# Optimization experiments

Hardware: AMD Instinct MI355X
Metric: run time of the kernel (lower is better)

## Reference

```python
import jax, jax.numpy as jnp
import numpy as np

D_MODEL = 2048
HIDDEN = 2048
NUM_EXPERTS = 8
TOP_K = 2
CAPACITY_FACTOR = 1.25


def setup_inputs() -> dict:
    key = jax.random.key(0)
    k1, k2, k3, k4, k5, k6 = jax.random.split(key, 6)
    N = 8192
    x = jax.random.normal(k1, (N, D_MODEL), dtype=jnp.float32)
    expert_weights = jax.random.uniform(k2, (N, TOP_K), dtype=jnp.float32)
    expert_indices = jax.random.randint(k3, (N, TOP_K), 0, NUM_EXPERTS)
    scale = 0.02
    w1 = jax.random.normal(k4, (NUM_EXPERTS, D_MODEL, HIDDEN), dtype=jnp.float32) * scale
    w3 = jax.random.normal(k5, (NUM_EXPERTS, D_MODEL, HIDDEN), dtype=jnp.float32) * scale
    w2 = jax.random.normal(k6, (NUM_EXPERTS, HIDDEN, D_MODEL), dtype=jnp.float32) * scale
    return {"x": x, "expert_weights": expert_weights, "expert_indices": expert_indices,
            "w1": w1, "w2": w2, "w3": w3}


def reference(x, expert_weights, expert_indices, w1, w2, w3):
    N, top_k = expert_weights.shape
    E = NUM_EXPERTS
    d = x.shape[-1]
    capacity = int(CAPACITY_FACTOR * top_k * N / E)  # expert_capacity()

    flat_idx = expert_indices.reshape(-1)            # (T,) T = N*top_k
    flat_w = expert_weights.reshape(-1)
    T = flat_idx.shape[0]

    # indices_and_bins: histogram + sort (jnp.argsort is stable)
    counts = jax.ops.segment_sum(jnp.ones((T,), dtype=jnp.int32), flat_idx, num_segments=E)
    order = jnp.argsort(flat_idx)                    # sorted assignment order
    sorted_e = flat_idx[order]                       # expert id per sorted slot
    starts = jnp.concatenate([jnp.zeros((1,), jnp.int32), jnp.cumsum(counts)[:-1].astype(jnp.int32)])
    off = jnp.arange(T, dtype=jnp.int32) - starts[sorted_e]  # position within expert bin
    valid = off < capacity                           # capacity dropping
    off_c = jnp.where(valid, off, 0)
    tok = order // top_k                             # source token per assignment

    # binned_gather -> (E, capacity, d); dropped/unfilled slots are zero
    xg = jnp.zeros((E, capacity, d), dtype=x.dtype)
    xg = xg.at[sorted_e, off_c].add(x[tok] * valid[:, None].astype(x.dtype))

    # per-expert SwiGLU MLP (grouped GEMMs)
    h = jax.nn.silu(jnp.einsum('ecd,edh->ech', xg, w1)) * jnp.einsum('ecd,edh->ech', xg, w3)
    y = jnp.einsum('ech,ehd->ecd', h, w2)

    # binned_scatter with expert_weights (weighted combine back to tokens)
    vals = y[sorted_e, off_c] * (flat_w[order] * valid.astype(x.dtype))[:, None]
    out = jnp.zeros((N, d), dtype=x.dtype).at[tok].add(vals)
    return out, counts
```

## Files before the change

kernel.cpp:

```cpp
#include <hip/hip_runtime.h>
#include <hip/hip_bf16.h>
#include <stdint.h>

#define NTOK 8192
#define DM 2048
#define DH 2048
#define NEXP 8
#define TOPK 2
#define TASSIGN (NTOK * TOPK)
#define CAP 2560
#define MROWS (NEXP * CAP)
#define BMTILES 10

using bf16x8 = __attribute__((ext_vector_type(8))) __bf16;
using bf16x2 = __attribute__((ext_vector_type(2))) __bf16;
using f32x4  = __attribute__((ext_vector_type(4))) float;

__device__ __forceinline__ void load_lds16(const void* g, void* l) {
    __builtin_amdgcn_global_load_lds((const __attribute__((address_space(1))) void*)g,
                                     (__attribute__((address_space(3))) void*)l,
                                     16, 0, 0);
}

__global__ void routing_kernel(const int* __restrict__ eidx,
                               int* __restrict__ counts,
                               int* __restrict__ slot_token,
                               int* __restrict__ assign_slot,
                               float* __restrict__ counts_out)
{
    __shared__ int base[NEXP];
    __shared__ int wcnt[4][NEXP];
    int tid = threadIdx.x, lane = tid & 63, wid = tid >> 6;
    for (int i = tid; i < MROWS; i += 256) slot_token[i] = -1;
    if (tid < NEXP) base[tid] = 0;
    __syncthreads();
    for (int t0 = 0; t0 < TASSIGN; t0 += 256) {
        int t = t0 + tid;
        int e = eidx[t];
        unsigned long long mymask = 0;
        #pragma unroll
        for (int ex = 0; ex < NEXP; ex++) {
            unsigned long long m = __ballot(e == ex);
            if (ex == e) mymask = m;
            if (lane == 0) wcnt[wid][ex] = __popcll(m);
        }
        int rankw = __popcll(mymask & ((1ull << lane) - 1ull));
        __syncthreads();
        int prev = base[e];
        for (int w = 0; w < wid; w++) prev += wcnt[w][e];
        int r = prev + rankw;
        int slot = (r < CAP) ? (e * CAP + r) : -1;
        assign_slot[t] = slot;
        if (slot >= 0) slot_token[slot] = t >> 1;
        __syncthreads();
        if (tid < NEXP) {
            int s = 0;
            for (int w = 0; w < 4; w++) s += wcnt[w][tid];
            base[tid] += s;
        }
        __syncthreads();
    }
    if (tid < NEXP) {
        counts[tid] = base[tid];
        counts_out[tid] = (float)base[tid];
    }
}

__global__ void transpose_kernel(const float* __restrict__ wa,
                                 const float* __restrict__ wb,
                                 const float* __restrict__ wc,
                                 __bf16* __restrict__ wat,
                                 __bf16* __restrict__ wbt,
                                 __bf16* __restrict__ wct)
{
    __shared__ float tile[64][65];
    int z = blockIdx.z;
    int mat = z >> 3, e = z & 7;
    const float* src = (mat == 0 ? wa : mat == 1 ? wb : wc) + (size_t)e * DM * DH;
    __bf16* dst = (mat == 0 ? wat : mat == 1 ? wbt : wct) + (size_t)e * DM * DH;
    int k0 = blockIdx.x * 64, n0 = blockIdx.y * 64;
    int tid = threadIdx.x;
    #pragma unroll
    for (int i = 0; i < 16; i++) {
        int lin = tid + i * 256;
        int r = lin >> 6, c = lin & 63;
        tile[r][c] = src[(size_t)(k0 + r) * DH + (n0 + c)];
    }
    __syncthreads();
    #pragma unroll
    for (int i = 0; i < 8; i++) {
        int lin = tid + i * 256;
        int r = lin >> 5, p = lin & 31;
        int c = p * 2;
        bf16x2 v;
        v[0] = (__bf16)tile[c][r];
        v[1] = (__bf16)tile[c + 1][r];
        *(bf16x2*)(dst + (size_t)(n0 + r) * DM + (k0 + c)) = v;
    }
}

__global__ void gather_kernel(const float* __restrict__ x,
                              const int* __restrict__ slot_token,
                              __bf16* __restrict__ xg)
{
    int slot = blockIdx.x;
    int tok = slot_token[slot];
    int c = threadIdx.x * 8;
    float f[8];
    if (tok >= 0) {
        const float4* px = (const float4*)(x + (size_t)tok * DM + c);
        float4 a = px[0], b = px[1];
        f[0] = a.x; f[1] = a.y; f[2] = a.z; f[3] = a.w;
        f[4] = b.x; f[5] = b.y; f[6] = b.z; f[7] = b.w;
    } else {
        #pragma unroll
        for (int i = 0; i < 8; i++) f[i] = 0.f;
    }
    bf16x8 v;
    #pragma unroll
    for (int i = 0; i < 8; i++) v[i] = (__bf16)f[i];
    *(bf16x8*)(xg + (size_t)slot * DM + c) = v;
}

template<bool FUSED>
__global__ __launch_bounds__(512, 2)
void gemm8_kernel(const __bf16* __restrict__ A,
                  const __bf16* __restrict__ B1,
                  const __bf16* __restrict__ B2,
                  __bf16* __restrict__ C,
                  const int* __restrict__ counts)
{
    constexpr int K = 2048, N = 2048;
    constexpr int BM = 256;
    constexpr int BN = FUSED ? 128 : 256;
    constexpr int NT = K / 64;
    constexpr int NJ = FUSED ? 2 : 4;
    constexpr int ROWB = K * 2;

    extern __shared__ char smem[];

    int mtile = blockIdx.x, ntile = blockIdx.y;
    int e = mtile / BMTILES;
    int mloc = (mtile % BMTILES) * BM;
    int rows = counts[e]; if (rows > CAP) rows = CAP;
    if (mloc >= rows) return;

    int tid = threadIdx.x;
    int wid = tid >> 6, lane = tid & 63;
    int wm = wid & 1, wn = wid >> 1;
    size_t rowBase = (size_t)e * CAP + mloc;

    int r0 = tid >> 3;
    int sw = ((tid & 7) ^ (r0 & 7)) << 4;
    const char* sA = (const char*)(A + (rowBase + r0) * (size_t)K) + sw;
    const char* sBu0; const char* sBu1;
    {
        size_t brow = (size_t)e * N + (size_t)ntile * BN + r0;
        sBu0 = (const char*)(B1 + brow * (size_t)K) + sw;
        if constexpr (FUSED) sBu1 = (const char*)(B2 + brow * (size_t)K) + sw;
        else                 sBu1 = sBu0 + 128 * ROWB;
    }
    char* lw = smem + wid * 1024;

    auto stage2 = [&](const char* s, int koff, int ldsOff) {
        load_lds16(s + koff, lw + ldsOff);
        load_lds16(s + koff + 64 * ROWB, lw + ldsOff + 8192);
    };

    int xc0 = (((lane >> 4) + 0) ^ (lane & 7)) << 4;
    int xc1 = (((lane >> 4) + 4) ^ (lane & 7)) << 4;
    int aOff = (wm * 128 + (lane & 15)) * 128;
    int bOff1, bOff2 = 0;
    if constexpr (FUSED) {
        bOff1 = 32768 + (wn * 32 + (lane & 15)) * 128;
        bOff2 = bOff1 + 16384;
    } else {
        bOff1 = 32768 + (wn * 64 + (lane & 15)) * 128;
    }

    f32x4 acc1[8][NJ];
    f32x4 acc2[FUSED ? 8 : 1][NJ];
    #pragma unroll
    for (int i = 0; i < 8; i++)
        #pragma unroll
        for (int j = 0; j < NJ; j++) {
            acc1[i][j] = (f32x4){0.f, 0.f, 0.f, 0.f};
            if constexpr (FUSED) acc2[i][j] = (f32x4){0.f, 0.f, 0.f, 0.f};
        }

    stage2(sA,              0, 0);
    stage2(sA + 128 * ROWB, 0, 16384);
    stage2(sBu0,            0, 32768);
    stage2(sBu1,            0, 49152);
    stage2(sBu0,          128, 65536 + 32768);
    stage2(sBu1,          128, 65536 + 49152);
    asm volatile("s_waitcnt vmcnt(4)" ::: "memory");
    __builtin_amdgcn_sched_barrier(0);
    __builtin_amdgcn_s_barrier();

    bf16x8 b1f[NJ][2];
    bf16x8 b2f[FUSED ? NJ : 1][2];

    #pragma unroll 2
    for (int t = 0; t < NT; ++t) {
        int bufC = (t & 1) << 16;
        int bufO = bufC ^ 65536;
        #pragma unroll
        for (int p = 0; p < 4; ++p) {
            bf16x8 a[2][2];
            #pragma unroll
            for (int i2 = 0; i2 < 2; ++i2) {
                const char* ap = smem + bufC + aOff + (2 * p + i2) * 2048;
                a[i2][0] = *(const bf16x8*)(ap + xc0);
                a[i2][1] = *(const bf16x8*)(ap + xc1);
            }
            if (p == 0) {
                #pragma unroll
                for (int j = 0; j < NJ; ++j) {
                    const char* bp = smem + bufC + bOff1 + j * 2048;
                    b1f[j][0] = *(const bf16x8*)(bp + xc0);
                    b1f[j][1] = *(const bf16x8*)(bp + xc1);
                    if constexpr (FUSED) {
                        const char* bp2 = smem + bufC + bOff2 + j * 2048;
                        b2f[j][0] = *(const bf16x8*)(bp2 + xc0);
                        b2f[j][1] = *(const bf16x8*)(bp2 + xc1);
                    }
                }
            }
            if (p == 0)      { if (t + 1 < NT) stage2(sA,              (t + 1) * 128, bufO); }
            else if (p == 1) { if (t + 1 < NT) stage2(sA + 128 * ROWB, (t + 1) * 128, bufO + 16384); }
            else if (p == 2) { if (t + 2 < NT) stage2(sBu0,            (t + 2) * 128, bufC + 32768); }
            else             { if (t + 2 < NT) stage2(sBu1,            (t + 2) * 128, bufC + 49152); }

            __builtin_amdgcn_s_barrier();
            asm volatile("s_waitcnt lgkmcnt(0)" ::: "memory");
            __builtin_amdgcn_sched_barrier(0);
            __builtin_amdgcn_s_setprio(1);
            #pragma unroll
            for (int ks = 0; ks < 2; ++ks)
                #pragma unroll
                for (int i2 = 0; i2 < 2; ++i2)
                    #pragma unroll
                    for (int j = 0; j < NJ; ++j) {
                        acc1[2 * p + i2][j] = __builtin_amdgcn_mfma_f32_16x16x32_bf16(
                            a[i2][ks], b1f[j][ks], acc1[2 * p + i2][j], 0, 0, 0);
                        if constexpr (FUSED)
                            acc2[2 * p + i2][j] = __builtin_amdgcn_mfma_f32_16x16x32_bf16(
                                a[i2][ks], b2f[j][ks], acc2[2 * p + i2][j], 0, 0, 0);
                    }
            __builtin_amdgcn_s_setprio(0);
            __builtin_amdgcn_sched_barrier(0);
            if (p == 3) {
                if (t + 2 < NT)      { asm volatile("s_waitcnt vmcnt(4)" ::: "memory"); }
                else if (t + 1 < NT) { asm volatile("s_waitcnt vmcnt(0)" ::: "memory"); }
                __builtin_amdgcn_sched_barrier(0);
            }
            __builtin_amdgcn_s_barrier();
        }
    }

    size_t crow0 = rowBase + wm * 128 + ((lane >> 4) << 2);
    int col0 = ntile * BN + wn * (FUSED ? 32 : 64) + (lane & 15);
    #pragma unroll
    for (int i = 0; i < 8; ++i)
        #pragma unroll
        for (int j = 0; j < NJ; ++j)
            #pragma unroll
            for (int r = 0; r < 4; ++r) {
                float v = acc1[i][j][r];
                if constexpr (FUSED) {
                    float z3 = acc2[i][j][r];
                    v = (v / (1.f + __expf(-v))) * z3;
                }
                C[(crow0 + i * 16 + r) * (size_t)N + (col0 + j * 16)] = (__bf16)v;
            }
}

__global__ void combine_kernel(const __bf16* __restrict__ y,
                               const int* __restrict__ assign_slot,
                               const float* __restrict__ ew,
                               float* __restrict__ out)
{
    int n = blockIdx.x;
    int s0 = assign_slot[2 * n], s1 = assign_slot[2 * n + 1];
    float w0 = ew[2 * n], w1 = ew[2 * n + 1];
    int c = threadIdx.x * 8;
    float acc[8];
    #pragma unroll
    for (int i = 0; i < 8; i++) acc[i] = 0.f;
    if (s0 >= 0) {
        bf16x8 v = *(const bf16x8*)(y + (size_t)s0 * DM + c);
        #pragma unroll
        for (int i = 0; i < 8; i++) acc[i] += w0 * (float)v[i];
    }
    if (s1 >= 0) {
        bf16x8 v = *(const bf16x8*)(y + (size_t)s1 * DM + c);
        #pragma unroll
        for (int i = 0; i < 8; i++) acc[i] += w1 * (float)v[i];
    }
    float4* po = (float4*)(out + (size_t)n * DM + c);
    po[0] = (float4){acc[0], acc[1], acc[2], acc[3]};
    po[1] = (float4){acc[4], acc[5], acc[6], acc[7]};
}

extern "C" void kernel_launch(void* const* d_in, const int* in_sizes, int n_in,
                              void* d_out, int out_size, void* d_ws, size_t ws_size,
                              hipStream_t stream)
{
    const float* x  = (const float*)d_in[0];
    const float* ew = (const float*)d_in[1];
    const int* eidx = (const int*)d_in[2];
    const float* w1 = (const float*)d_in[3];
    const float* w2 = (const float*)d_in[4];
    const float* w3 = (const float*)d_in[5];
    float* out = (float*)d_out;
    float* counts_out = out + (size_t)NTOK * DM;

    char* ws = (char*)d_ws;
    size_t off = 0;
    auto alloc = [&](size_t bytes) -> void* {
        off = (off + 255) & ~(size_t)255;
        void* p = ws + off;
        off += bytes;
        return p;
    };
    int* slot_token  = (int*)alloc((size_t)MROWS * 4);
    int* assign_slot = (int*)alloc((size_t)TASSIGN * 4);
    int* counts      = (int*)alloc(NEXP * 4);
    __bf16* xg  = (__bf16*)alloc((size_t)MROWS * DM * 2);
    __bf16* h   = (__bf16*)alloc((size_t)MROWS * DH * 2);
    __bf16* w1t = (__bf16*)alloc((size_t)NEXP * DM * DH * 2);
    __bf16* w3t = (__bf16*)alloc((size_t)NEXP * DM * DH * 2);
    __bf16* w2t = (__bf16*)alloc((size_t)NEXP * DM * DH * 2);
    __bf16* y = xg;

    static int attr_done = 0;
    if (!attr_done) {
        hipFuncSetAttribute((const void*)gemm8_kernel<true>,
                            hipFuncAttributeMaxDynamicSharedMemorySize, 131072);
        hipFuncSetAttribute((const void*)gemm8_kernel<false>,
                            hipFuncAttributeMaxDynamicSharedMemorySize, 131072);
        attr_done = 1;
    }

    routing_kernel<<<1, 256, 0, stream>>>(eidx, counts, slot_token, assign_slot, counts_out);
    transpose_kernel<<<dim3(32, 32, 24), 256, 0, stream>>>(w1, w3, w2, w1t, w3t, w2t);
    gather_kernel<<<MROWS, 256, 0, stream>>>(x, slot_token, xg);
    gemm8_kernel<true><<<dim3(NEXP * BMTILES, 16), 512, 131072, stream>>>(xg, w1t, w3t, h, counts);
    gemm8_kernel<false><<<dim3(NEXP * BMTILES, 8), 512, 131072, stream>>>(h, w2t, nullptr, y, counts);
    combine_kernel<<<NTOK, 256, 0, stream>>>(y, assign_slot, ew, out);
}
```

Baseline: 995.9 us.

## Parallelize routing, vectorize transpose stores, remap GEMM blocks per XCD, reorder prefetch

Routing moves from one serial 256-thread block to three kernels: a per-chunk histogram, a scan, and a per-chunk assign, so it runs across many blocks instead of looping 64 times with barriers. The weight transpose now writes 16-byte bf16x8 vectors instead of 4-byte pairs. GEMM blocks are launched on a 1D grid and remapped so each group of blockIdx%8 (likely one XCD) gets a contiguous range of tiles for one expert, which should improve L2 reuse of weights. The A-tile prefetches are also merged into the first phase. The cost is two extra kernel launches, and the prefetch reorder changes how the vmcnt waits line up.

```diff
diff --git a/kernel.cpp b/kernel.cpp
--- a/kernel.cpp
+++ b/kernel.cpp
@@ -11,9 +11,9 @@
 #define CAP 2560
 #define MROWS (NEXP * CAP)
 #define BMTILES 10
+#define RBLK 64
 
 using bf16x8 = __attribute__((ext_vector_type(8))) __bf16;
-using bf16x2 = __attribute__((ext_vector_type(2))) __bf16;
 using f32x4  = __attribute__((ext_vector_type(4))) float;
 
 __device__ __forceinline__ void load_lds16(const void* g, void* l) {
@@ -22,48 +22,68 @@
                                      16, 0, 0);
 }
 
-__global__ void routing_kernel(const int* __restrict__ eidx,
-                               int* __restrict__ counts,
-                               int* __restrict__ slot_token,
-                               int* __restrict__ assign_slot,
-                               float* __restrict__ counts_out)
-{
-    __shared__ int base[NEXP];
+__global__ void route_hist_kernel(const int* __restrict__ eidx,
+                                  int* __restrict__ chunk_cnt,
+                                  int* __restrict__ slot_token)
+{
+    int b = blockIdx.x, tid = threadIdx.x, lane = tid & 63, wid = tid >> 6;
     __shared__ int wcnt[4][NEXP];
-    int tid = threadIdx.x, lane = tid & 63, wid = tid >> 6;
-    for (int i = tid; i < MROWS; i += 256) slot_token[i] = -1;
-    if (tid < NEXP) base[tid] = 0;
+    for (int i = b * 320 + tid; i < (b + 1) * 320; i += 256) slot_token[i] = -1;
+    int e = eidx[b * 256 + tid];
+    #pragma unroll
+    for (int ex = 0; ex < NEXP; ex++) {
+        unsigned long long m = __ballot(e == ex);
+        if (lane == 0) wcnt[wid][ex] = __popcll(m);
+    }
     __syncthreads();
-    for (int t0 = 0; t0 < TASSIGN; t0 += 256) {
-        int t = t0 + tid;
-        int e = eidx[t];
-        unsigned long long mymask = 0;
-        #pragma unroll
-        for (int ex = 0; ex < NEXP; ex++) {
-            unsigned long long m = __ballot(e == ex);
-            if (ex == e) mymask = m;
-            if (lane == 0) wcnt[wid][ex] = __popcll(m);
+    if (tid < NEXP) {
+        int s = 0;
+        #pragma unroll
+        for (int w = 0; w < 4; w++) s += wcnt[w][tid];
+        chunk_cnt[b * NEXP + tid] = s;
+    }
+}
+
+__global__ void route_scan_kernel(const int* __restrict__ chunk_cnt,
+                                  int* __restrict__ chunk_base,
+                                  int* __restrict__ counts,
+                                  float* __restrict__ counts_out)
+{
+    int e = threadIdx.x;
+    if (e < NEXP) {
+        int run = 0;
+        for (int b = 0; b < RBLK; b++) {
+            chunk_base[b * NEXP + e] = run;
+            run += chunk_cnt[b * NEXP + e];
         }
-        int rankw = __popcll(mymask & ((1ull << lane) - 1ull));
-        __syncthreads();
-        int prev = base[e];
-        for (int w = 0; w < wid; w++) prev += wcnt[w][e];
-        int r = prev + rankw;
-        int slot = (r < CAP) ? (e * CAP + r) : -1;
-        assign_slot[t] = slot;
-        if (slot >= 0) slot_token[slot] = t >> 1;
-        __syncthreads();
-        if (tid < NEXP) {
-            int s = 0;
-            for (int w = 0; w < 4; w++) s += wcnt[w][tid];
-            base[tid] += s;
-        }
-        __syncthreads();
-    }
-    if (tid < NEXP) {
-        counts[tid] = base[tid];
-        counts_out[tid] = (float)base[tid];
-    }
+        counts[e] = run;
+        counts_out[e] = (float)run;
+    }
+}
+
+__global__ void route_assign_kernel(const int* __restrict__ eidx,
+                                    const int* __restrict__ chunk_base,
+                                    int* __restrict__ slot_token,
+                                    int* __restrict__ assign_slot)
+{
+    int b = blockIdx.x, tid = threadIdx.x, lane = tid & 63, wid = tid >> 6;
+    __shared__ int wcnt[4][NEXP];
+    int t = b * 256 + tid;
+    int e = eidx[t];
+    unsigned long long mymask = 0;
+    #pragma unroll
+    for (int ex = 0; ex < NEXP; ex++) {
+        unsigned long long m = __ballot(e == ex);
+        if (ex == e) mymask = m;
+        if (lane == 0) wcnt[wid][ex] = __popcll(m);
+    }
+    int rankw = __popcll(mymask & ((1ull << lane) - 1ull));
+    __syncthreads();
+    int r = chunk_base[b * NEXP + e] + rankw;
+    for (int w = 0; w < wid; w++) r += wcnt[w][e];
+    int slot = (r < CAP) ? (e * CAP + r) : -1;
+    assign_slot[t] = slot;
+    if (slot >= 0) slot_token[slot] = t >> 1;
 }
 
 __global__ void transpose_kernel(const float* __restrict__ wa,
@@ -88,14 +108,13 @@
     }
     __syncthreads();
     #pragma unroll
-    for (int i = 0; i < 8; i++) {
-        int lin = tid + i * 256;
-        int r = lin >> 5, p = lin & 31;
-        int c = p * 2;
-        bf16x2 v;
-        v[0] = (__bf16)tile[c][r];
-        v[1] = (__bf16)tile[c + 1][r];
-        *(bf16x2*)(dst + (size_t)(n0 + r) * DM + (k0 + c)) = v;
+    for (int i = 0; i < 2; i++) {
+        int rn = (tid >> 3) + i * 32;
+        int ck = (tid & 7) * 8;
+        bf16x8 v;
+        #pragma unroll
+        for (int j = 0; j < 8; j++) v[j] = (__bf16)tile[ck + j][rn];
+        *(bf16x8*)(dst + (size_t)(n0 + rn) * DM + (k0 + ck)) = v;
     }
 }
 
@@ -133,15 +152,24 @@
     constexpr int K = 2048, N = 2048;
     constexpr int BM = 256;
     constexpr int BN = FUSED ? 128 : 256;
+    constexpr int NTILES = N / BN;
     constexpr int NT = K / 64;
     constexpr int NJ = FUSED ? 2 : 4;
     constexpr int ROWB = K * 2;
 
     extern __shared__ char smem[];
 
-    int mtile = blockIdx.x, ntile = blockIdx.y;
-    int e = mtile / BMTILES;
-    int mloc = (mtile % BMTILES) * BM;
+    constexpr int PERE = BMTILES * NTILES;
+    constexpr int PERX = NEXP * PERE / 8;
+    int w = (blockIdx.x % 8) * PERX + blockIdx.x / 8;
+    int e = w / PERE;
+    int r = w % PERE;
+    int ntg = r / (BMTILES * 4);
+    int rr  = r % (BMTILES * 4);
+    int ntile = ntg * 4 + rr / BMTILES;
+    int mtile = rr % BMTILES;
+
+    int mloc = mtile * BM;
     int rows = counts[e]; if (rows > CAP) rows = CAP;
     if (mloc >= rows) return;
 
@@ -227,10 +255,13 @@
                     }
                 }
             }
-            if (p == 0)      { if (t + 1 < NT) stage2(sA,              (t + 1) * 128, bufO); }
-            else if (p == 1) { if (t + 1 < NT) stage2(sA + 128 * ROWB, (t + 1) * 128, bufO + 16384); }
-            else if (p == 2) { if (t + 2 < NT) stage2(sBu0,            (t + 2) * 128, bufC + 32768); }
-            else             { if (t + 2 < NT) stage2(sBu1,            (t + 2) * 128, bufC + 49152); }
+            if (p == 0) {
+                if (t + 1 < NT) {
+                    stage2(sA,              (t + 1) * 128, bufO);
+                    stage2(sA + 128 * ROWB, (t + 1) * 128, bufO + 16384);
+                }
+            } else if (p == 1) { if (t + 2 < NT) stage2(sBu0, (t + 2) * 128, bufC + 32768); }
+            else if (p == 2)   { if (t + 2 < NT) stage2(sBu1, (t + 2) * 128, bufC + 49152); }
 
             __builtin_amdgcn_s_barrier();
             asm volatile("s_waitcnt lgkmcnt(0)" ::: "memory");
@@ -266,13 +297,13 @@
         #pragma unroll
         for (int j = 0; j < NJ; ++j)
             #pragma unroll
-            for (int r = 0; r < 4; ++r) {
-                float v = acc1[i][j][r];
+            for (int r4 = 0; r4 < 4; ++r4) {
+                float v = acc1[i][j][r4];
                 if constexpr (FUSED) {
-                    float z3 = acc2[i][j][r];
+                    float z3 = acc2[i][j][r4];
                     v = (v / (1.f + __expf(-v))) * z3;
                 }
-                C[(crow0 + i * 16 + r) * (size_t)N + (col0 + j * 16)] = (__bf16)v;
+                C[(crow0 + i * 16 + r4) * (size_t)N + (col0 + j * 16)] = (__bf16)v;
             }
 }
 
@@ -327,6 +358,8 @@
     int* slot_token  = (int*)alloc((size_t)MROWS * 4);
     int* assign_slot = (int*)alloc((size_t)TASSIGN * 4);
     int* counts      = (int*)alloc(NEXP * 4);
+    int* chunk_cnt   = (int*)alloc((size_t)RBLK * NEXP * 4);
+    int* chunk_base  = (int*)alloc((size_t)RBLK * NEXP * 4);
     __bf16* xg  = (__bf16*)alloc((size_t)MROWS * DM * 2);
     __bf16* h   = (__bf16*)alloc((size_t)MROWS * DH * 2);
     __bf16* w1t = (__bf16*)alloc((size_t)NEXP * DM * DH * 2);
@@ -343,10 +376,12 @@
         attr_done = 1;
     }
 
-    routing_kernel<<<1, 256, 0, stream>>>(eidx, counts, slot_token, assign_slot, counts_out);
+    route_hist_kernel<<<RBLK, 256, 0, stream>>>(eidx, chunk_cnt, slot_token);
+    route_scan_kernel<<<1, 64, 0, stream>>>(chunk_cnt, chunk_base, counts, counts_out);
+    route_assign_kernel<<<RBLK, 256, 0, stream>>>(eidx, chunk_base, slot_token, assign_slot);
     transpose_kernel<<<dim3(32, 32, 24), 256, 0, stream>>>(w1, w3, w2, w1t, w3t, w2t);
     gather_kernel<<<MROWS, 256, 0, stream>>>(x, slot_token, xg);
-    gemm8_kernel<true><<<dim3(NEXP * BMTILES, 16), 512, 131072, stream>>>(xg, w1t, w3t, h, counts);
-    gemm8_kernel<false><<<dim3(NEXP * BMTILES, 8), 512, 131072, stream>>>(h, w2t, nullptr, y, counts);
+    gemm8_kernel<true><<<NEXP * BMTILES * 16, 512, 131072, stream>>>(xg, w1t, w3t, h, counts);
+    gemm8_kernel<false><<<NEXP * BMTILES * 8, 512, 131072, stream>>>(h, w2t, nullptr, y, counts);
     combine_kernel<<<NTOK, 256, 0, stream>>>(y, assign_slot, ew, out);
 }
```

Measured after the change: 923.1 us. -7.3%, faster.
